# Performance work log

Measured on AMD Instinct MI355X. Metric: run time of the kernel, lower is better.

The kernel has to match this reference:

```python
import jax, jax.numpy as jnp
import numpy as np
from jax import lax

B, C, L = 2048, 9605, 8
WL_PER_LABEL = 50
ALPHA = 0.5        # training_config['alpha4']
ALPHA1 = 0.1       # margin
ALPHA2 = 2.0       # training_config['alpha2']
ALPHA3 = 10.0      # training_config['alpha3']
ALPHA_OTHER = 0.5
NEG = jnp.float32(-1e30)


def setup_inputs() -> dict:
    key = jax.random.key(0)
    k1, k2, k3, k4 = jax.random.split(key, 4)
    x = jax.random.normal(k1, (B, C), dtype=jnp.float32) * 2.0
    y = (jax.random.uniform(k2, (B, C)) < 0.005).astype(jnp.float32)
    y_neg = (jax.random.uniform(k3, (B, C)) < 0.005).astype(jnp.float32)
    # whitelist masks: L app-labels, each whitelisting ~WL_PER_LABEL raw classes
    idx = jax.random.randint(k4, (L, WL_PER_LABEL), 0, C)
    wl_masks = jnp.zeros((L, C), dtype=bool).at[jnp.arange(L)[:, None], idx].set(True)
    return {"x": x, "y": y, "y_neg": y_neg, "wl_masks": wl_masks}


def reference(x, y, y_neg, wl_masks):
    # y_neg is consumed by the original forward (find_gt_whitelist) but never
    # affects the returned loss, faithfully ignored here.
    xs_pos = jax.nn.sigmoid(x)                                  # [B, C]
    # top_k_thres = max(11th-largest sigmoid, alpha_other)
    thres = jnp.maximum(lax.top_k(xs_pos, 11)[0][:, 10], ALPHA_OTHER)  # [B]
    # per-label whitelist max: m[b,l] = max_{c in wl_l} xs_pos[b,c]
    m = jnp.max(jnp.where(wl_masks[None, :, :], xs_pos[:, None, :], NEG), axis=-1)  # [B, L]
    # label l is a ground-truth whitelist label iff y has any positive in wl_l
    has_pos = jnp.einsum('bc,lc->bl', y, wl_masks.astype(y.dtype)) > 0   # [B, L]
    correct_max = jnp.max(jnp.where(has_pos, m, NEG), axis=-1)           # [B]
    incorrect_max = jnp.max(jnp.where(~has_pos, m, NEG), axis=-1)        # [B]
    any_correct = jnp.any(has_pos, axis=-1)
    any_incorrect = jnp.any(~has_pos, axis=-1)
    # union whitelist max (the "other" branch uses xs_pos over all wl indices)
    union_max = jnp.max(jnp.where(jnp.any(wl_masks, axis=0)[None, :], xs_pos, NEG), axis=-1)
    x1 = jnp.where(any_correct, correct_max, thres)
    x2 = jnp.where(any_correct,
                   jnp.where(any_incorrect, jnp.maximum(incorrect_max, thres), thres),
                   union_max)
    coef = jnp.where(any_correct, 1.0, 1.0 - ALPHA)
    d = x2 - x1 + ALPHA1
    rank = jnp.where(d > 0, ALPHA2, 1.0) * jax.nn.sigmoid(ALPHA3 * d)
    return jnp.mean(coef * rank)
```

## Files before the change

### kernel.cpp

```cpp
#include <hip/hip_runtime.h>

#define CC 9605
#define BB 2048
#define LL 8
#define NSLOT 41
#define CAND_MAX 2048
#define NEGF (-1e30f)

#define WS_PARTIALS_OFF 16384

__device__ __forceinline__ unsigned enc_f(float f) {
  unsigned u = __float_as_uint(f);
  return (u & 0x80000000u) ? ~u : (u | 0x80000000u);
}
__device__ __forceinline__ float dec_u(unsigned e) {
  unsigned u = (e & 0x80000000u) ? (e & 0x7fffffffu) : ~e;
  return __uint_as_float(u);
}
__device__ __forceinline__ float sigm(float z) {
  return 1.0f / (1.0f + __expf(-z));
}

__global__ void wl_sniff(const unsigned char* __restrict__ wl,
                         unsigned* __restrict__ wsu) {
  const int stride = gridDim.x * blockDim.x;
  unsigned f = 0u;
  for (int j = blockIdx.x * blockDim.x + threadIdx.x; j < LL * CC; j += stride) {
    unsigned b = wl[j];
    if (b == 1u)    { f |= 2u; if ((j & 3) != 0) f |= 1u; }
    if (b == 0x3fu) { f |= 8u; if ((j & 3) == 1) f |= 4u; }
  }
#pragma unroll
  for (int off = 32; off >= 1; off >>= 1) f |= __shfl_xor(f, off, 64);
  if ((threadIdx.x & 63) == 0 && f) atomicOr(&wsu[1], f);
}

__global__ void wl_compact(const unsigned char* __restrict__ wl,
                           unsigned* __restrict__ wsu) {
  const int tid = threadIdx.x;
  const int lane = tid & 63;
  const int c = blockIdx.x * 256 + tid;
  const unsigned g = wsu[1];
  const int dt = (g & 1u) ? 0 : (g & 4u) ? 3 : (g & 2u) ? 1 : (g & 8u) ? 2 : 0;
  const int* wl32 = (const int*)wl;
  const float* wlf = (const float*)wl;
  const unsigned short* wlh = (const unsigned short*)wl;
  unsigned m = 0u;
  if (c < CC) {
#pragma unroll
    for (int l = 0; l < LL; ++l) {
      int j = l * CC + c;
      bool on;
      if (dt == 0) on = (wl[j] != 0);
      else if (dt == 1) on = (wl32[j] != 0);
      else if (dt == 2) on = (wlf[j] != 0.0f);
      else on = (wlh[j] != 0);
      if (on) m |= (1u << l);
    }
  }
  unsigned long long bal = __ballot(m != 0u);
  if (bal) {
    unsigned wcnt = (unsigned)__popcll(bal);
    unsigned basep = 0u;
    if (lane == 0) basep = atomicAdd(&wsu[0], wcnt);
    basep = __shfl(basep, 0, 64);
    if (m) {
      unsigned pos = basep + (unsigned)__popcll(bal & ((1ull << lane) - 1ull));
      if (pos < 2048u) wsu[4 + pos] = ((unsigned)c << 8) | m;
    }
  }
}

__global__ __launch_bounds__(256) void loss_kernel(
    const float* __restrict__ x, const float* __restrict__ y,
    const unsigned* __restrict__ wsu, float* __restrict__ partials) {
  __shared__ unsigned sh_hist[256];
  __shared__ unsigned sh_cand[CAND_MAX];
  __shared__ unsigned sh_redU[4];
  __shared__ unsigned sh_sel[2];
  __shared__ float sh_wl[4][12];

  const int tid = threadIdx.x;
  const int lane = tid & 63;
  const int wid = tid >> 6;
  const int b = blockIdx.x;
  const long long base = (long long)b * CC;

  unsigned enc[NSLOT];
  const int soff = (4 - (b & 3)) & 3;
  const int ngroups = (CC - soff) >> 2;
  const int tailn = CC - soff - (ngroups << 2);
  const int m_extra = soff + tailn;
  const float4* vp = (const float4*)(x + base + soff);
#pragma unroll
  for (int i = 0; i < 10; ++i) {
    int g = tid + (i << 8);
    if (g < ngroups) {
      float4 v = vp[g];
      enc[4 * i + 0] = enc_f(v.x);
      enc[4 * i + 1] = enc_f(v.y);
      enc[4 * i + 2] = enc_f(v.z);
      enc[4 * i + 3] = enc_f(v.w);
    } else {
      enc[4 * i + 0] = 0u; enc[4 * i + 1] = 0u;
      enc[4 * i + 2] = 0u; enc[4 * i + 3] = 0u;
    }
  }
  if (tid < m_extra) {
    int col = (tid < soff) ? tid : (soff + (ngroups << 2) + (tid - soff));
    enc[40] = enc_f(x[base + col]);
  } else {
    enc[40] = 0u;
  }

  unsigned mx = 0u;
#pragma unroll
  for (int i = 0; i < NSLOT; ++i) mx = max(mx, enc[i]);

  auto blk_count = [&](unsigned T) -> unsigned {
    unsigned cnt = 0u;
#pragma unroll
    for (int i = 0; i < NSLOT; ++i) cnt += (enc[i] >= T) ? 1u : 0u;
#pragma unroll
    for (int off = 32; off >= 1; off >>= 1) cnt += __shfl_xor(cnt, off, 64);
    __syncthreads();
    if (lane == 0) sh_redU[wid] = cnt;
    __syncthreads();
    return sh_redU[0] + sh_redU[1] + sh_redU[2] + sh_redU[3];
  };

#pragma unroll
  for (int off = 32; off >= 1; off >>= 1) mx = max(mx, __shfl_xor(mx, off, 64));
  if (lane == 0) sh_redU[wid] = mx;
  __syncthreads();
  const unsigned Emax =
      max(max(sh_redU[0], sh_redU[1]), max(sh_redU[2], sh_redU[3]));

  unsigned E11 = 0u;
  bool done = false;
  unsigned c = blk_count(Emax);
  if (c >= 11u) { E11 = Emax; done = true; }
  unsigned lo = Emax, hi = Emax;
  if (!done) {
    const unsigned STEP = 1u << 23;
    while (true) {
      hi = lo;
      lo = (lo > STEP) ? (lo - STEP) : 1u;
      c = blk_count(lo);
      if (c >= 11u) break;
      if (lo == 1u) break;
    }
    while (c > CAND_MAX) {
      if (hi - lo <= 1u) { E11 = lo; done = true; break; }
      unsigned mid = lo + ((hi - lo) >> 1);
      unsigned cm = blk_count(mid);
      if (cm >= 11u) { lo = mid; c = cm; } else { hi = mid; }
    }
  }

  if (!done) {
    __syncthreads();
    if (tid == 0) sh_sel[0] = 0u;
    __syncthreads();
#pragma unroll
    for (int i = 0; i < NSLOT; ++i) {
      bool pr = (enc[i] >= lo);
      unsigned long long bal = __ballot(pr);
      if (bal) {
        unsigned wcnt = (unsigned)__popcll(bal);
        unsigned basep = 0u;
        if (lane == 0) basep = atomicAdd(&sh_sel[0], wcnt);
        basep = __shfl(basep, 0, 64);
        if (pr) {
          unsigned posn = basep + (unsigned)__popcll(bal & ((1ull << lane) - 1ull));
          sh_cand[posn] = enc[i];
        }
      }
    }
    __syncthreads();

    unsigned prefix = 0u, r = 11u;
    for (int p = 3; p >= 0; --p) {
      sh_hist[tid] = 0u;
      __syncthreads();
      for (unsigned i = tid; i < c; i += 256u) {
        unsigned e = sh_cand[i];
        bool match =
            (p == 3) || ((e >> ((p + 1) * 8)) == (prefix >> ((p + 1) * 8)));
        if (match) atomicAdd(&sh_hist[(e >> (p * 8)) & 255u], 1u);
      }
      __syncthreads();
      if (wid == 0) {
        unsigned b0 = sh_hist[4 * lane + 0], b1 = sh_hist[4 * lane + 1];
        unsigned b2 = sh_hist[4 * lane + 2], b3 = sh_hist[4 * lane + 3];
        unsigned s = b0 + b1 + b2 + b3;
        unsigned t = s;
#pragma unroll
        for (int off = 1; off < 64; off <<= 1) {
          unsigned v = __shfl_down(t, off, 64);
          if (lane + off < 64) t += v;
        }
        unsigned above = t - s;
        unsigned suf3 = above + b3, suf2 = suf3 + b2, suf1 = suf2 + b1,
                 suf0 = suf1 + b0;
        if (suf0 >= r && suf1 < r) { sh_sel[0] = 4u * lane + 0u; sh_sel[1] = r - suf1; }
        if (suf1 >= r && suf2 < r) { sh_sel[0] = 4u * lane + 1u; sh_sel[1] = r - suf2; }
        if (suf2 >= r && suf3 < r) { sh_sel[0] = 4u * lane + 2u; sh_sel[1] = r - suf3; }
        if (suf3 >= r && above < r){ sh_sel[0] = 4u * lane + 3u; sh_sel[1] = r - above; }
      }
      __syncthreads();
      prefix |= sh_sel[0] << (p * 8);
      r = sh_sel[1];
    }
    E11 = prefix;
  }

  __syncthreads();
  const unsigned nu = wsu[0];
  const unsigned* ents = wsu + 4;
  float lm[8];
#pragma unroll
  for (int l = 0; l < 8; ++l) lm[l] = NEGF;
  float um = NEGF;
  unsigned present = 0u, posm = 0u;
  for (unsigned e = tid; e < nu; e += 256u) {
    unsigned ent = ents[e];
    unsigned ccol = ent >> 8;
    unsigned mk = ent & 255u;
    float xv = x[base + (long long)ccol];
    float yv = y[base + (long long)ccol];
    present |= mk;
    if (yv > 0.0f) posm |= mk;
    um = fmaxf(um, xv);
#pragma unroll
    for (int l = 0; l < 8; ++l)
      if ((mk >> l) & 1u) lm[l] = fmaxf(lm[l], xv);
  }
#pragma unroll
  for (int off = 32; off >= 1; off >>= 1) {
    um = fmaxf(um, __shfl_xor(um, off, 64));
    present |= __shfl_xor(present, off, 64);
    posm |= __shfl_xor(posm, off, 64);
#pragma unroll
    for (int l = 0; l < 8; ++l) lm[l] = fmaxf(lm[l], __shfl_xor(lm[l], off, 64));
  }
  if (lane == 0) {
#pragma unroll
    for (int l = 0; l < 8; ++l) sh_wl[wid][l] = lm[l];
    sh_wl[wid][8] = um;
    sh_wl[wid][9] = __uint_as_float(present);
    sh_wl[wid][10] = __uint_as_float(posm);
  }
  __syncthreads();

  if (tid == 0) {
    float LM[8], UM = NEGF;
    unsigned PR = 0u, PO = 0u;
#pragma unroll
    for (int l = 0; l < 8; ++l) LM[l] = NEGF;
    for (int w = 0; w < 4; ++w) {
#pragma unroll
      for (int l = 0; l < 8; ++l) LM[l] = fmaxf(LM[l], sh_wl[w][l]);
      UM = fmaxf(UM, sh_wl[w][8]);
      PR |= __float_as_uint(sh_wl[w][9]);
      PO |= __float_as_uint(sh_wl[w][10]);
    }
    float x11 = dec_u(E11);
    float thres = fmaxf(sigm(x11), 0.5f);
    float cmax = NEGF, imax = NEGF;
#pragma unroll
    for (int l = 0; l < 8; ++l) {
      float ml = ((PR >> l) & 1u) ? sigm(LM[l]) : NEGF;
      if ((PO >> l) & 1u) cmax = fmaxf(cmax, ml);
      else imax = fmaxf(imax, ml);
    }
    bool anyc = (PO != 0u);
    bool anyi = (PO != 255u);
    float unionmax = (nu > 0u) ? sigm(UM) : NEGF;
    float x1 = anyc ? cmax : thres;
    float x2 = anyc ? (anyi ? fmaxf(imax, thres) : thres) : unionmax;
    float coef = anyc ? 1.0f : 0.5f;
    float dd = x2 - x1 + 0.1f;
    float rank = ((dd > 0.0f) ? 2.0f : 1.0f) * sigm(10.0f * dd);
    partials[b] = coef * rank;
  }
}

__global__ void final_reduce(const float* __restrict__ partials,
                             float* __restrict__ out) {
  __shared__ float sh[4];
  const int tid = threadIdx.x;
  const int lane = tid & 63;
  const int wid = tid >> 6;
  float s = 0.0f;
  for (int i = tid; i < BB; i += 256) s += partials[i];
#pragma unroll
  for (int off = 32; off >= 1; off >>= 1) s += __shfl_xor(s, off, 64);
  if (lane == 0) sh[wid] = s;
  __syncthreads();
  if (tid == 0) out[0] = (sh[0] + sh[1] + sh[2] + sh[3]) * (1.0f / (float)BB);
}

extern "C" void kernel_launch(void* const* d_in, const int* in_sizes, int n_in,
                              void* d_out, int out_size, void* d_ws,
                              size_t ws_size, hipStream_t stream) {
  const float* x = (const float*)d_in[0];
  const float* y = (const float*)d_in[1];
  const unsigned char* wl = (const unsigned char*)d_in[3];
  float* out = (float*)d_out;
  unsigned* wsu = (unsigned*)d_ws;
  float* partials = (float*)((char*)d_ws + WS_PARTIALS_OFF);

  hipMemsetAsync(d_ws, 0, 16, stream);
  wl_sniff<<<64, 256, 0, stream>>>(wl, wsu);
  wl_compact<<<(CC + 255) / 256, 256, 0, stream>>>(wl, wsu);
  loss_kernel<<<BB, 256, 0, stream>>>(x, y, wsu, partials);
  final_reduce<<<1, 256, 0, stream>>>(partials, out);
}
```

Baseline: 236.5 us.

## Fuse final reduction into loss kernel and simplify top-11 selection

Folds the final mean reduction into the loss kernel through a last-block atomic counter, which removes one kernel launch. The four-pass radix histogram select is replaced by a brute-force rank count over at most 512 candidates, and CAND_MAX is lowered to match. The whitelist gather is moved ahead of the threshold search so its global loads overlap with that work, and the per-label and union masks are packed into one word. Also vectorises wl_sniff to read whole 32-bit words and adds a launch_bounds occupancy hint. The tradeoffs are a few extra bisection passes to shrink the candidate set, an O(c) loop per thread, and a last-block fence pattern for the final sum.

```diff
diff --git a/kernel.cpp b/kernel.cpp
--- a/kernel.cpp
+++ b/kernel.cpp
@@ -4,7 +4,7 @@
 #define BB 2048
 #define LL 8
 #define NSLOT 41
-#define CAND_MAX 2048
+#define CAND_MAX 512
 #define NEGF (-1e30f)
 
 #define WS_PARTIALS_OFF 16384
@@ -21,14 +21,19 @@
   return 1.0f / (1.0f + __expf(-z));
 }
 
-__global__ void wl_sniff(const unsigned char* __restrict__ wl,
+__global__ void wl_sniff(const unsigned* __restrict__ wlw,
                          unsigned* __restrict__ wsu) {
+  const int nwords = (LL * CC) / 4;
   const int stride = gridDim.x * blockDim.x;
   unsigned f = 0u;
-  for (int j = blockIdx.x * blockDim.x + threadIdx.x; j < LL * CC; j += stride) {
-    unsigned b = wl[j];
-    if (b == 1u)    { f |= 2u; if ((j & 3) != 0) f |= 1u; }
-    if (b == 0x3fu) { f |= 8u; if ((j & 3) == 1) f |= 4u; }
+  for (int j = blockIdx.x * blockDim.x + threadIdx.x; j < nwords; j += stride) {
+    unsigned w = wlw[j];
+#pragma unroll
+    for (int k = 0; k < 4; ++k) {
+      unsigned b = (w >> (8 * k)) & 255u;
+      if (b == 1u)    { f |= 2u; if (k != 0) f |= 1u; }
+      if (b == 0x3fu) { f |= 8u; if (k == 1) f |= 4u; }
+    }
   }
 #pragma unroll
   for (int off = 32; off >= 1; off >>= 1) f |= __shfl_xor(f, off, 64);
@@ -71,14 +76,18 @@
   }
 }
 
-__global__ __launch_bounds__(256) void loss_kernel(
+__global__ __launch_bounds__(256, 4) void loss_kernel(
     const float* __restrict__ x, const float* __restrict__ y,
-    const unsigned* __restrict__ wsu, float* __restrict__ partials) {
-  __shared__ unsigned sh_hist[256];
+    unsigned* __restrict__ wsu, float* __restrict__ partials,
+    float* __restrict__ out) {
   __shared__ unsigned sh_cand[CAND_MAX];
-  __shared__ unsigned sh_redU[4];
-  __shared__ unsigned sh_sel[2];
-  __shared__ float sh_wl[4][12];
+  __shared__ unsigned sh_redM[4];
+  __shared__ unsigned sh_redC[4];
+  __shared__ unsigned sh_cnt;
+  __shared__ unsigned sh_e11;
+  __shared__ unsigned sh_last;
+  __shared__ float sh_wl[4][10];
+  __shared__ float sh_fin[4];
 
   const int tid = threadIdx.x;
   const int lane = tid & 63;
@@ -93,17 +102,21 @@
   const int m_extra = soff + tailn;
   const float4* vp = (const float4*)(x + base + soff);
 #pragma unroll
-  for (int i = 0; i < 10; ++i) {
-    int g = tid + (i << 8);
+  for (int i = 0; i < 9; ++i) {
+    float4 v = vp[tid + (i << 8)];
+    enc[4 * i + 0] = enc_f(v.x);
+    enc[4 * i + 1] = enc_f(v.y);
+    enc[4 * i + 2] = enc_f(v.z);
+    enc[4 * i + 3] = enc_f(v.w);
+  }
+  {
+    int g = tid + (9 << 8);
     if (g < ngroups) {
       float4 v = vp[g];
-      enc[4 * i + 0] = enc_f(v.x);
-      enc[4 * i + 1] = enc_f(v.y);
-      enc[4 * i + 2] = enc_f(v.z);
-      enc[4 * i + 3] = enc_f(v.w);
+      enc[36] = enc_f(v.x); enc[37] = enc_f(v.y);
+      enc[38] = enc_f(v.z); enc[39] = enc_f(v.w);
     } else {
-      enc[4 * i + 0] = 0u; enc[4 * i + 1] = 0u;
-      enc[4 * i + 2] = 0u; enc[4 * i + 3] = 0u;
+      enc[36] = 0u; enc[37] = 0u; enc[38] = 0u; enc[39] = 0u;
     }
   }
   if (tid < m_extra) {
@@ -113,9 +126,35 @@
     enc[40] = 0u;
   }
 
+  const unsigned nu = wsu[0];
+  const unsigned* ents = wsu + 4;
+  float lm[8];
+#pragma unroll
+  for (int l = 0; l < 8; ++l) lm[l] = NEGF;
+  unsigned pmask = 0u;
+  for (unsigned e = tid; e < nu; e += 256u) {
+    unsigned ent = ents[e];
+    unsigned ccol = ent >> 8;
+    unsigned mk = ent & 255u;
+    float xv = x[base + (long long)ccol];
+    float yv = y[base + (long long)ccol];
+    pmask |= mk;
+    if (yv > 0.0f) pmask |= (mk << 8);
+#pragma unroll
+    for (int l = 0; l < 8; ++l)
+      if ((mk >> l) & 1u) lm[l] = fmaxf(lm[l], xv);
+  }
+
   unsigned mx = 0u;
 #pragma unroll
   for (int i = 0; i < NSLOT; ++i) mx = max(mx, enc[i]);
+#pragma unroll
+  for (int off = 32; off >= 1; off >>= 1) mx = max(mx, __shfl_xor(mx, off, 64));
+  if (lane == 0) sh_redM[wid] = mx;
+  if (tid == 0) { sh_cnt = 0u; }
+  __syncthreads();
+  const unsigned Emax =
+      max(max(sh_redM[0], sh_redM[1]), max(sh_redM[2], sh_redM[3]));
 
   auto blk_count = [&](unsigned T) -> unsigned {
     unsigned cnt = 0u;
@@ -124,44 +163,29 @@
 #pragma unroll
     for (int off = 32; off >= 1; off >>= 1) cnt += __shfl_xor(cnt, off, 64);
     __syncthreads();
-    if (lane == 0) sh_redU[wid] = cnt;
-    __syncthreads();
-    return sh_redU[0] + sh_redU[1] + sh_redU[2] + sh_redU[3];
+    if (lane == 0) sh_redC[wid] = cnt;
+    __syncthreads();
+    return sh_redC[0] + sh_redC[1] + sh_redC[2] + sh_redC[3];
   };
-
-#pragma unroll
-  for (int off = 32; off >= 1; off >>= 1) mx = max(mx, __shfl_xor(mx, off, 64));
-  if (lane == 0) sh_redU[wid] = mx;
-  __syncthreads();
-  const unsigned Emax =
-      max(max(sh_redU[0], sh_redU[1]), max(sh_redU[2], sh_redU[3]));
 
   unsigned E11 = 0u;
   bool done = false;
-  unsigned c = blk_count(Emax);
-  if (c >= 11u) { E11 = Emax; done = true; }
-  unsigned lo = Emax, hi = Emax;
+  unsigned lo = (Emax > (1u << 23)) ? (Emax - (1u << 23)) : 1u;
+  unsigned hi = Emax + 1u;
+  unsigned c = blk_count(lo);
+  while (c < 11u && lo > 1u) {
+    hi = lo;
+    lo = (lo > (1u << 23)) ? (lo - (1u << 23)) : 1u;
+    c = blk_count(lo);
+  }
+  while (c > CAND_MAX) {
+    if (hi - lo <= 1u) { E11 = lo; done = true; break; }
+    unsigned mid = lo + ((hi - lo) >> 1);
+    unsigned cm = blk_count(mid);
+    if (cm >= 11u) { lo = mid; c = cm; } else { hi = mid; }
+  }
+
   if (!done) {
-    const unsigned STEP = 1u << 23;
-    while (true) {
-      hi = lo;
-      lo = (lo > STEP) ? (lo - STEP) : 1u;
-      c = blk_count(lo);
-      if (c >= 11u) break;
-      if (lo == 1u) break;
-    }
-    while (c > CAND_MAX) {
-      if (hi - lo <= 1u) { E11 = lo; done = true; break; }
-      unsigned mid = lo + ((hi - lo) >> 1);
-      unsigned cm = blk_count(mid);
-      if (cm >= 11u) { lo = mid; c = cm; } else { hi = mid; }
-    }
-  }
-
-  if (!done) {
-    __syncthreads();
-    if (tid == 0) sh_sel[0] = 0u;
-    __syncthreads();
 #pragma unroll
     for (int i = 0; i < NSLOT; ++i) {
       bool pr = (enc[i] >= lo);
@@ -169,7 +193,7 @@
       if (bal) {
         unsigned wcnt = (unsigned)__popcll(bal);
         unsigned basep = 0u;
-        if (lane == 0) basep = atomicAdd(&sh_sel[0], wcnt);
+        if (lane == 0) basep = atomicAdd(&sh_cnt, wcnt);
         basep = __shfl(basep, 0, 64);
         if (pr) {
           unsigned posn = basep + (unsigned)__popcll(bal & ((1ull << lane) - 1ull));
@@ -178,127 +202,83 @@
       }
     }
     __syncthreads();
-
-    unsigned prefix = 0u, r = 11u;
-    for (int p = 3; p >= 0; --p) {
-      sh_hist[tid] = 0u;
-      __syncthreads();
-      for (unsigned i = tid; i < c; i += 256u) {
-        unsigned e = sh_cand[i];
-        bool match =
-            (p == 3) || ((e >> ((p + 1) * 8)) == (prefix >> ((p + 1) * 8)));
-        if (match) atomicAdd(&sh_hist[(e >> (p * 8)) & 255u], 1u);
-      }
-      __syncthreads();
-      if (wid == 0) {
-        unsigned b0 = sh_hist[4 * lane + 0], b1 = sh_hist[4 * lane + 1];
-        unsigned b2 = sh_hist[4 * lane + 2], b3 = sh_hist[4 * lane + 3];
-        unsigned s = b0 + b1 + b2 + b3;
-        unsigned t = s;
-#pragma unroll
-        for (int off = 1; off < 64; off <<= 1) {
-          unsigned v = __shfl_down(t, off, 64);
-          if (lane + off < 64) t += v;
-        }
-        unsigned above = t - s;
-        unsigned suf3 = above + b3, suf2 = suf3 + b2, suf1 = suf2 + b1,
-                 suf0 = suf1 + b0;
-        if (suf0 >= r && suf1 < r) { sh_sel[0] = 4u * lane + 0u; sh_sel[1] = r - suf1; }
-        if (suf1 >= r && suf2 < r) { sh_sel[0] = 4u * lane + 1u; sh_sel[1] = r - suf2; }
-        if (suf2 >= r && suf3 < r) { sh_sel[0] = 4u * lane + 2u; sh_sel[1] = r - suf3; }
-        if (suf3 >= r && above < r){ sh_sel[0] = 4u * lane + 3u; sh_sel[1] = r - above; }
-      }
-      __syncthreads();
-      prefix |= sh_sel[0] << (p * 8);
-      r = sh_sel[1];
-    }
-    E11 = prefix;
-  }
-
+    unsigned e0 = (tid < (int)c) ? sh_cand[tid] : 0u;
+    unsigned e1 = (tid + 256 < (int)c) ? sh_cand[tid + 256] : 0u;
+    unsigned gt0 = 0u, ge0 = 0u, gt1 = 0u, ge1 = 0u;
+    for (unsigned j = 0; j < c; ++j) {
+      unsigned v = sh_cand[j];
+      gt0 += (v > e0); ge0 += (v >= e0);
+      gt1 += (v > e1); ge1 += (v >= e1);
+    }
+    if (tid < (int)c && gt0 <= 10u && ge0 >= 11u) sh_e11 = e0;
+    if (tid + 256 < (int)c && gt1 <= 10u && ge1 >= 11u) sh_e11 = e1;
+    __syncthreads();
+    E11 = sh_e11;
+  }
+
+#pragma unroll
+  for (int off = 32; off >= 1; off >>= 1) {
+    pmask |= __shfl_xor(pmask, off, 64);
+#pragma unroll
+    for (int l = 0; l < 8; ++l) lm[l] = fmaxf(lm[l], __shfl_xor(lm[l], off, 64));
+  }
+  if (lane == 0) {
+#pragma unroll
+    for (int l = 0; l < 8; ++l) sh_wl[wid][l] = lm[l];
+    sh_wl[wid][8] = __uint_as_float(pmask);
+  }
   __syncthreads();
-  const unsigned nu = wsu[0];
-  const unsigned* ents = wsu + 4;
-  float lm[8];
-#pragma unroll
-  for (int l = 0; l < 8; ++l) lm[l] = NEGF;
-  float um = NEGF;
-  unsigned present = 0u, posm = 0u;
-  for (unsigned e = tid; e < nu; e += 256u) {
-    unsigned ent = ents[e];
-    unsigned ccol = ent >> 8;
-    unsigned mk = ent & 255u;
-    float xv = x[base + (long long)ccol];
-    float yv = y[base + (long long)ccol];
-    present |= mk;
-    if (yv > 0.0f) posm |= mk;
-    um = fmaxf(um, xv);
-#pragma unroll
-    for (int l = 0; l < 8; ++l)
-      if ((mk >> l) & 1u) lm[l] = fmaxf(lm[l], xv);
-  }
-#pragma unroll
-  for (int off = 32; off >= 1; off >>= 1) {
-    um = fmaxf(um, __shfl_xor(um, off, 64));
-    present |= __shfl_xor(present, off, 64);
-    posm |= __shfl_xor(posm, off, 64);
-#pragma unroll
-    for (int l = 0; l < 8; ++l) lm[l] = fmaxf(lm[l], __shfl_xor(lm[l], off, 64));
-  }
-  if (lane == 0) {
-#pragma unroll
-    for (int l = 0; l < 8; ++l) sh_wl[wid][l] = lm[l];
-    sh_wl[wid][8] = um;
-    sh_wl[wid][9] = __uint_as_float(present);
-    sh_wl[wid][10] = __uint_as_float(posm);
-  }
-  __syncthreads();
 
   if (tid == 0) {
-    float LM[8], UM = NEGF;
-    unsigned PR = 0u, PO = 0u;
+    float LM[8];
+    unsigned PM = 0u;
 #pragma unroll
     for (int l = 0; l < 8; ++l) LM[l] = NEGF;
     for (int w = 0; w < 4; ++w) {
 #pragma unroll
       for (int l = 0; l < 8; ++l) LM[l] = fmaxf(LM[l], sh_wl[w][l]);
-      UM = fmaxf(UM, sh_wl[w][8]);
-      PR |= __float_as_uint(sh_wl[w][9]);
-      PO |= __float_as_uint(sh_wl[w][10]);
-    }
-    float x11 = dec_u(E11);
-    float thres = fmaxf(sigm(x11), 0.5f);
-    float cmax = NEGF, imax = NEGF;
+      PM |= __float_as_uint(sh_wl[w][8]);
+    }
+    unsigned PR = PM & 255u, PO = (PM >> 8) & 255u;
+    float thres = fmaxf(sigm(dec_u(E11)), 0.5f);
+    float cmax = NEGF, imax = NEGF, umax = NEGF;
 #pragma unroll
     for (int l = 0; l < 8; ++l) {
-      float ml = ((PR >> l) & 1u) ? sigm(LM[l]) : NEGF;
-      if ((PO >> l) & 1u) cmax = fmaxf(cmax, ml);
-      else imax = fmaxf(imax, ml);
+      if ((PR >> l) & 1u) {
+        float ml = sigm(LM[l]);
+        umax = fmaxf(umax, ml);
+        if ((PO >> l) & 1u) cmax = fmaxf(cmax, ml);
+        else imax = fmaxf(imax, ml);
+      } else if (!((PO >> l) & 1u)) {
+        imax = fmaxf(imax, NEGF);
+      }
     }
     bool anyc = (PO != 0u);
     bool anyi = (PO != 255u);
-    float unionmax = (nu > 0u) ? sigm(UM) : NEGF;
     float x1 = anyc ? cmax : thres;
-    float x2 = anyc ? (anyi ? fmaxf(imax, thres) : thres) : unionmax;
+    float x2 = anyc ? (anyi ? fmaxf(imax, thres) : thres)
+                    : ((nu > 0u) ? umax : NEGF);
     float coef = anyc ? 1.0f : 0.5f;
     float dd = x2 - x1 + 0.1f;
     float rank = ((dd > 0.0f) ? 2.0f : 1.0f) * sigm(10.0f * dd);
     partials[b] = coef * rank;
-  }
-}
-
-__global__ void final_reduce(const float* __restrict__ partials,
-                             float* __restrict__ out) {
-  __shared__ float sh[4];
-  const int tid = threadIdx.x;
-  const int lane = tid & 63;
-  const int wid = tid >> 6;
-  float s = 0.0f;
-  for (int i = tid; i < BB; i += 256) s += partials[i];
-#pragma unroll
-  for (int off = 32; off >= 1; off >>= 1) s += __shfl_xor(s, off, 64);
-  if (lane == 0) sh[wid] = s;
+    __threadfence();
+    unsigned old = atomicAdd(&wsu[2], 1u);
+    sh_last = (old == (unsigned)(BB - 1)) ? 1u : 0u;
+  }
   __syncthreads();
-  if (tid == 0) out[0] = (sh[0] + sh[1] + sh[2] + sh[3]) * (1.0f / (float)BB);
+
+  if (sh_last) {
+    __threadfence();
+    float s = 0.0f;
+    for (int i = tid; i < BB; i += 256) s += partials[i];
+#pragma unroll
+    for (int off = 32; off >= 1; off >>= 1) s += __shfl_xor(s, off, 64);
+    if (lane == 0) sh_fin[wid] = s;
+    __syncthreads();
+    if (tid == 0)
+      out[0] = (sh_fin[0] + sh_fin[1] + sh_fin[2] + sh_fin[3]) * (1.0f / (float)BB);
+  }
 }
 
 extern "C" void kernel_launch(void* const* d_in, const int* in_sizes, int n_in,
@@ -312,8 +292,7 @@
   float* partials = (float*)((char*)d_ws + WS_PARTIALS_OFF);
 
   hipMemsetAsync(d_ws, 0, 16, stream);
-  wl_sniff<<<64, 256, 0, stream>>>(wl, wsu);
+  wl_sniff<<<64, 256, 0, stream>>>((const unsigned*)wl, wsu);
   wl_compact<<<(CC + 255) / 256, 256, 0, stream>>>(wl, wsu);
-  loss_kernel<<<BB, 256, 0, stream>>>(x, y, wsu, partials);
-  final_reduce<<<1, 256, 0, stream>>>(partials, out);
-}
+  loss_kernel<<<BB, 256, 0, stream>>>(x, y, wsu, partials, out);
+}
```

Measured after the change: 321.7 us. 1.36x slower.
